# Kernel optimization log

Measured on AMD Instinct MI355X. Metric: run time of the kernel, lower is better.

## Reference

```python
import jax, jax.numpy as jnp
import numpy as np

B, S, D = 2, 2048, 2048
H, G, HD = 16, 8, 128          # query heads, kv groups, head_dim
GS = H // G                     # group size (queries per kv head)
EPS = 1e-6


def _rmsnorm(x, scale):
    # Qwen3-compatible: upcast to f32, rms over last dim, scale
    xf = x.astype(jnp.float32)
    ms = jnp.mean(xf * xf, axis=-1, keepdims=True)
    return (xf * jax.lax.rsqrt(ms + EPS) * scale).astype(x.dtype)


def _rope(x, cos, sin):
    # x: (b, h, s, hd); cos/sin: (s, hd) rotate-half convention
    hd = x.shape[-1]
    x1, x2 = x[..., : hd // 2], x[..., hd // 2 :]
    rotated = jnp.concatenate([-x2, x1], axis=-1)
    s = x.shape[2]
    c = cos[None, None, :s, :]
    sn = sin[None, None, :s, :]
    return (x * c + rotated * sn).astype(x.dtype)


def setup_inputs() -> dict:
    key = jax.random.key(0)
    ks = jax.random.split(key, 8)
    x = jax.random.normal(ks[0], (B, S, D), jnp.float32)
    # causal mask: True = masked (future positions)
    mask = jnp.triu(jnp.ones((S, S), dtype=bool), k=1)
    # RoPE tables, rotate-half convention (cat(angles, angles))
    inv_freq = 1.0 / (10000.0 ** (np.arange(0, HD, 2, dtype=np.float32) / HD))
    angles = np.arange(S, dtype=np.float32)[:, None] * inv_freq[None, :]
    angles = np.concatenate([angles, angles], axis=-1)  # (S, HD)
    cos = jnp.asarray(np.cos(angles))
    sin = jnp.asarray(np.sin(angles))
    std = 0.02
    Wq = jax.random.normal(ks[1], (D, H * HD), jnp.float32) * std
    Wk = jax.random.normal(ks[2], (D, G * HD), jnp.float32) * std
    Wv = jax.random.normal(ks[3], (D, G * HD), jnp.float32) * std
    Wo = jax.random.normal(ks[4], (H * HD, D), jnp.float32) * std
    q_scale = jnp.ones((HD,), jnp.float32)
    k_scale = jnp.ones((HD,), jnp.float32)
    return {"x": x, "mask": mask, "cos": cos, "sin": sin,
            "Wq": Wq, "Wk": Wk, "Wv": Wv, "Wo": Wo,
            "q_scale": q_scale, "k_scale": k_scale}


def reference(x, mask, cos, sin, Wq, Wk, Wv, Wo, q_scale, k_scale):
    b, s, _ = x.shape
    q = (x @ Wq).reshape(b, s, H, HD).transpose(0, 2, 1, 3)   # (b,H,s,hd)
    k = (x @ Wk).reshape(b, s, G, HD).transpose(0, 2, 1, 3)   # (b,G,s,hd)
    v = (x @ Wv).reshape(b, s, G, HD).transpose(0, 2, 1, 3)   # (b,G,s,hd)
    q = _rmsnorm(q, q_scale)
    k = _rmsnorm(k, k_scale)
    q = _rope(q, cos, sin)
    k = _rope(k, cos, sin)
    # grouped attention: avoid repeat_interleave by grouping query heads
    qg = q.reshape(b, G, GS, s, HD)
    scores = jnp.einsum('bghqd,bgkd->bghqk', qg, k)           # (b,G,GS,s,s)
    scores = jnp.where(mask[None, None, None, :, :], -jnp.inf, scores)
    weights = jax.nn.softmax(scores / jnp.sqrt(jnp.float32(HD)), axis=-1)
    ctx = jnp.einsum('bghqk,bgkd->bghqd', weights, v)          # (b,G,GS,s,hd)
    ctx = ctx.reshape(b, H, s, HD).transpose(0, 2, 1, 3).reshape(b, s, H * HD)
    return ctx @ Wo
```

## Files before the change

### kernel.cpp

```cpp
#include <hip/hip_runtime.h>
#include <stdint.h>

#define S_LEN 2048
#define NH 16
#define NG 8
#define HDIM 128

typedef __bf16 bf16x8 __attribute__((ext_vector_type(8)));
typedef __bf16 bf16x4v __attribute__((ext_vector_type(4)));
typedef float f32x4 __attribute__((ext_vector_type(4)));

#define MFMA16(a, b, c) __builtin_amdgcn_mfma_f32_16x16x32_bf16((a), (b), (c), 0, 0, 0)

__device__ __forceinline__ uint16_t f2bf(float f) {
  union { float f; uint32_t u; } v; v.f = f;
  return (uint16_t)((v.u + 0x7fffu + ((v.u >> 16) & 1u)) >> 16);
}

__device__ __forceinline__ void gload16(const void* g, void* l) {
  __builtin_amdgcn_global_load_lds(
      (__attribute__((address_space(1))) const void*)g,
      (__attribute__((address_space(3))) void*)l, 16, 0, 0);
}

__global__ __launch_bounds__(256) void cvt_x_kernel(
    const float* __restrict__ x, uint16_t* __restrict__ xb, int n4) {
  int i = blockIdx.x * 256 + threadIdx.x;
  if (i >= n4) return;
  float4 v = ((const float4*)x)[i];
  ushort4 o;
  o.x = f2bf(v.x); o.y = f2bf(v.y); o.z = f2bf(v.z); o.w = f2bf(v.w);
  ((ushort4*)xb)[i] = o;
}

__global__ __launch_bounds__(256) void trans_cvt_kernel(
    const float* __restrict__ src, uint16_t* __restrict__ dst, int K, int N) {
  __shared__ float T[32][33];
  int n0 = blockIdx.x * 32, k0 = blockIdx.y * 32;
  int tx = threadIdx.x & 31, ty = threadIdx.x >> 5;
  #pragma unroll
  for (int i = 0; i < 4; ++i)
    T[ty + i * 8][tx] = src[(size_t)(k0 + ty + i * 8) * N + n0 + tx];
  __syncthreads();
  #pragma unroll
  for (int i = 0; i < 4; ++i)
    dst[(size_t)(n0 + ty + i * 8) * K + k0 + tx] = f2bf(T[tx][ty + i * 8]);
}

template <int NISSUE>
__device__ __forceinline__ void stage_half(const uint16_t* __restrict__ g,
                                           int ldg, char* lds, int tid) {
  #pragma unroll
  for (int i = 0; i < NISSUE; ++i) {
    int ch = i * 512 + tid;
    int pair = ch >> 3, slotd = ch & 7;
    int slotl = slotd ^ (pair & 7);
    int row = pair * 2 + (slotl >> 2), c2 = slotl & 3;
    gload16(g + (size_t)row * ldg + c2 * 8, lds + ch * 16);
  }
}

__device__ __forceinline__ bf16x8 ldsfrag(const char* half_base, int row, int l4) {
  int pair = row >> 1;
  int slot = ((row & 1) << 2) | l4;
  return *(const bf16x8*)(half_base + pair * 128 + ((slot ^ (pair & 7)) * 16));
}

#define BAR() asm volatile("s_barrier" ::: "memory")

template <int BM>
__global__ __launch_bounds__(512, 2) void gemm8p_kernel(
    const uint16_t* __restrict__ A, const uint16_t* __restrict__ BT,
    float* __restrict__ C, int M, int N, int K, int gridN) {
  extern __shared__ char smem[];
  constexpr int MI = BM / 32;
  constexpr int LA = BM / 128;
  constexpr int ABYTES = BM * 64;
  const int tid = threadIdx.x, lane = tid & 63;
  const int wid = tid >> 6;
  const int l15 = lane & 15, l4 = lane >> 4;
  const int wm = wid >> 2, wn = wid & 3;

  const int nwg = gridDim.x, bid = blockIdx.x;
  const int cpx = nwg >> 3;
  const int swz = (bid & 7) * cpx + (bid >> 3);
  const int m0 = (swz / gridN) * BM, n0 = (swz % gridN) * 256;

  const uint16_t* Ag = A + (size_t)m0 * K;
  const uint16_t* Bg = BT + (size_t)n0 * K;
  const int NT = K >> 6;

#define ABASE(p, k) (smem + (((p) << 1) | (k)) * ABYTES)
#define BBASE(p, k) (smem + 4 * ABYTES + (((p) << 1) | (k)) * 16384)

  f32x4 acc[MI][4];
  #pragma unroll
  for (int mi = 0; mi < MI; ++mi)
    #pragma unroll
    for (int ni = 0; ni < 4; ++ni) acc[mi][ni] = (f32x4){0.f, 0.f, 0.f, 0.f};

  stage_half<LA>(Ag, K, ABASE(0, 0), tid);
  stage_half<2>(Bg, K, BBASE(0, 0), tid);
  stage_half<LA>(Ag + 32, K, ABASE(0, 1), tid);
  stage_half<2>(Bg + 32, K, BBASE(0, 1), tid);
  stage_half<LA>(Ag + 64, K, ABASE(1, 0), tid);
  stage_half<2>(Bg + 64, K, BBASE(1, 0), tid);
  if constexpr (BM == 256) asm volatile("s_waitcnt vmcnt(4)" ::: "memory");
  else                     asm volatile("s_waitcnt vmcnt(3)" ::: "memory");
  BAR();

  int par = 0;
  const int arow = wm * (BM / 2) + l15;
  for (int u = 0; u < NT; ++u, par ^= 1) {
    const int k0 = u * 64;
    bf16x8 af[MI], bf0, bf1;
    #pragma unroll
    for (int mi = 0; mi < MI; ++mi) af[mi] = ldsfrag(ABASE(par, 0), arow + mi * 16, l4);
    bf0 = ldsfrag(BBASE(par, 0), wn * 64 + l15, l4);
    bf1 = ldsfrag(BBASE(par, 0), wn * 64 + 16 + l15, l4);
    if (u + 1 < NT) stage_half<LA>(Ag + (k0 + 96), K, ABASE(par ^ 1, 1), tid);
    BAR();
    __builtin_amdgcn_s_setprio(1);
    #pragma unroll
    for (int mi = 0; mi < MI; ++mi) {
      acc[mi][0] = MFMA16(af[mi], bf0, acc[mi][0]);
      acc[mi][1] = MFMA16(af[mi], bf1, acc[mi][1]);
    }
    __builtin_amdgcn_s_setprio(0);
    BAR();
    bf0 = ldsfrag(BBASE(par, 0), wn * 64 + 32 + l15, l4);
    bf1 = ldsfrag(BBASE(par, 0), wn * 64 + 48 + l15, l4);
    if (u + 1 < NT) stage_half<2>(Bg + (k0 + 96), K, BBASE(par ^ 1, 1), tid);
    BAR();
    __builtin_amdgcn_s_setprio(1);
    #pragma unroll
    for (int mi = 0; mi < MI; ++mi) {
      acc[mi][2] = MFMA16(af[mi], bf0, acc[mi][2]);
      acc[mi][3] = MFMA16(af[mi], bf1, acc[mi][3]);
    }
    __builtin_amdgcn_s_setprio(0);
    BAR();
    #pragma unroll
    for (int mi = 0; mi < MI; ++mi) af[mi] = ldsfrag(ABASE(par, 1), arow + mi * 16, l4);
    bf0 = ldsfrag(BBASE(par, 1), wn * 64 + 32 + l15, l4);
    bf1 = ldsfrag(BBASE(par, 1), wn * 64 + 48 + l15, l4);
    if (u + 2 < NT) stage_half<LA>(Ag + (k0 + 128), K, ABASE(par, 0), tid);
    BAR();
    __builtin_amdgcn_s_setprio(1);
    #pragma unroll
    for (int mi = 0; mi < MI; ++mi) {
      acc[mi][2] = MFMA16(af[mi], bf0, acc[mi][2]);
      acc[mi][3] = MFMA16(af[mi], bf1, acc[mi][3]);
    }
    __builtin_amdgcn_s_setprio(0);
    BAR();
    bf0 = ldsfrag(BBASE(par, 1), wn * 64 + l15, l4);
    bf1 = ldsfrag(BBASE(par, 1), wn * 64 + 16 + l15, l4);
    if (u + 2 < NT) stage_half<2>(Bg + (k0 + 128), K, BBASE(par, 0), tid);
    BAR();
    __builtin_amdgcn_s_setprio(1);
    #pragma unroll
    for (int mi = 0; mi < MI; ++mi) {
      acc[mi][0] = MFMA16(af[mi], bf0, acc[mi][0]);
      acc[mi][1] = MFMA16(af[mi], bf1, acc[mi][1]);
    }
    __builtin_amdgcn_s_setprio(0);
    if (u + 2 < NT) {
      if constexpr (BM == 256) asm volatile("s_waitcnt vmcnt(4)" ::: "memory");
      else                     asm volatile("s_waitcnt vmcnt(3)" ::: "memory");
    } else {
      asm volatile("s_waitcnt vmcnt(0)" ::: "memory");
    }
    BAR();
  }

  #pragma unroll
  for (int mi = 0; mi < MI; ++mi)
    #pragma unroll
    for (int ni = 0; ni < 4; ++ni) {
      float* dst = C + (size_t)(m0 + wm * (BM / 2) + mi * 16 + l4 * 4) * N +
                   n0 + wn * 64 + ni * 16 + l15;
      #pragma unroll
      for (int r = 0; r < 4; ++r) dst[(size_t)r * N] = acc[mi][ni][r];
    }
#undef ABASE
#undef BBASE
}

__global__ __launch_bounds__(256) void qk_rope_kernel(
    const float* __restrict__ QKV, const float* __restrict__ cosb,
    const float* __restrict__ sinb, const float* __restrict__ qs,
    const float* __restrict__ ks, uint16_t* __restrict__ Qb,
    uint16_t* __restrict__ Kb) {
  const int task = blockIdx.x * 4 + (threadIdx.x >> 6);
  const int lane = threadIdx.x & 63;
  const int hh = task % 24;
  const int row = task / 24;
  const int s = row & (S_LEN - 1);
  const int b = row >> 11;
  const float c1 = cosb[s * 128 + lane], c2 = cosb[s * 128 + 64 + lane];
  const float s1 = sinb[s * 128 + lane], s2 = sinb[s * 128 + 64 + lane];
  const float* src = QKV + (size_t)row * 4096;
  float v1, v2, sc1, sc2, outscale;
  uint16_t* dst;
  if (hh < 16) {
    v1 = src[hh * 128 + lane]; v2 = src[hh * 128 + 64 + lane];
    sc1 = qs[lane]; sc2 = qs[lane + 64];
    outscale = 0.088388347648318447f;
    dst = Qb + ((size_t)(b * NH + hh) * S_LEN + s) * 128;
  } else {
    int g = hh - 16;
    v1 = src[2048 + g * 128 + lane]; v2 = src[2048 + g * 128 + 64 + lane];
    sc1 = ks[lane]; sc2 = ks[lane + 64];
    outscale = 1.0f;
    dst = Kb + ((size_t)(b * NG + g) * S_LEN + s) * 128;
  }
  float ss = v1 * v1 + v2 * v2;
  #pragma unroll
  for (int o = 1; o < 64; o <<= 1) ss += __shfl_xor(ss, o);
  float inv = rsqrtf(ss * (1.0f / 128.0f) + 1e-6f);
  float n1 = v1 * inv * sc1, n2 = v2 * inv * sc2;
  dst[lane] = f2bf((n1 * c1 - n2 * s1) * outscale);
  dst[lane + 64] = f2bf((n2 * c2 + n1 * s2) * outscale);
}

__global__ __launch_bounds__(256) void v_trans_kernel(
    const float* __restrict__ QKV, uint16_t* __restrict__ Vt) {
  __shared__ uint16_t T[128][72];
  const int s0 = blockIdx.x * 64;
  const int bg = blockIdx.y;
  const int b = bg >> 3, g = bg & 7;
  const int tid = threadIdx.x;
  const int tc = tid & 127, tr = tid >> 7;
  const float* src = QKV + ((size_t)(b * S_LEN + s0)) * 4096 + 3072 + g * 128;
  #pragma unroll
  for (int i = 0; i < 32; ++i) {
    int r = i * 2 + tr;
    T[tc][r] = f2bf(src[(size_t)r * 4096 + tc]);
  }
  __syncthreads();
  uint16_t* dst = Vt + (size_t)bg * 128 * S_LEN + s0;
  #pragma unroll
  for (int i = 0; i < 32; ++i) {
    int idx = i * 256 + tid;
    int d = idx >> 6, sof = idx & 63;
    dst[(size_t)d * S_LEN + sof] = T[d][sof];
  }
}

__global__ __launch_bounds__(512) void attn_kernel(
    const uint16_t* __restrict__ Qb, const uint16_t* __restrict__ Kb,
    const uint16_t* __restrict__ Vt, uint16_t* __restrict__ Ctx) {
  __shared__ uint8_t smem[65536 + 8 * 2304];
  const int tid = threadIdx.x, lane = tid & 63, wid = tid >> 6;
  uint16_t* Ps = (uint16_t*)(smem + 65536) + wid * 1152;
  const int l15 = lane & 15, l4 = lane >> 4;

  const int bg = blockIdx.y;
  const int b = bg >> 3, g = bg & 7;
  const int h = (g << 1) | (wid >> 2);
  const int bh = b * NH + h;

  const uint16_t* Qh = Qb + (size_t)bh * S_LEN * HDIM;
  const uint16_t* Kh = Kb + (size_t)bg * S_LEN * HDIM;
  const uint16_t* Vh = Vt + (size_t)bg * HDIM * S_LEN;

  const int k_row = lane >> 4, k_c = lane & 15;
  const int v_row = lane >> 3, v_c = lane & 7;

#define STAGE(kt_, buf_)                                                      \
  do {                                                                        \
    const int kv0_ = (kt_) * 64;                                              \
    uint16_t* KsB_ = (uint16_t*)(smem + (buf_) * 16384);                      \
    uint16_t* VsB_ = (uint16_t*)(smem + 32768 + (buf_) * 16384);              \
    _Pragma("unroll")                                                         \
    for (int i_ = 0; i_ < 2; ++i_) {                                          \
      int chunk_ = wid * 2 + i_;                                              \
      int row_ = chunk_ * 4 + k_row;                                          \
      int sc_ = (k_c ^ (row_ & 7)) * 8;                                       \
      gload16(Kh + (size_t)(kv0_ + row_) * HDIM + sc_, KsB_ + chunk_ * 512);  \
    }                                                                         \
    _Pragma("unroll")                                                         \
    for (int i_ = 0; i_ < 2; ++i_) {                                          \
      int chunk_ = wid * 2 + i_;                                              \
      int row_ = chunk_ * 8 + v_row;                                          \
      int sc_ = (v_c ^ (row_ & 7)) * 8;                                       \
      gload16(Vh + (size_t)row_ * S_LEN + kv0_ + sc_, VsB_ + chunk_ * 512);   \
    }                                                                         \
  } while (0)

  for (int half = 0; half < 2; ++half) {
    const int qtile = half ? (31 - (int)blockIdx.x) : (int)blockIdx.x;
    const int q0 = qtile * 64;
    const int qrow = q0 + (wid & 3) * 16 + l15;

    bf16x8 qf[4];
    #pragma unroll
    for (int kk = 0; kk < 4; ++kk)
      qf[kk] = *(const bf16x8*)(Qh + (size_t)qrow * HDIM + kk * 32 + l4 * 8);

    f32x4 acc[8];
    #pragma unroll
    for (int i = 0; i < 8; ++i) acc[i] = (f32x4){0.f, 0.f, 0.f, 0.f};
    float mrun = -1e30f, lrun = 0.f;

    const int nt = qtile + 1;
    int cur = 0;
    STAGE(0, 0);
    asm volatile("s_waitcnt vmcnt(0)\ns_barrier" ::: "memory");

    for (int kt = 0; kt < nt; ++kt) {
      const int kv0 = kt * 64;
      if (kt + 1 < nt) STAGE(kt + 1, cur ^ 1);

      uint16_t* Ks = (uint16_t*)(smem + cur * 16384);
      uint16_t* Vs = (uint16_t*)(smem + 32768 + cur * 16384);

      f32x4 sc[4];
      #pragma unroll
      for (int i = 0; i < 4; ++i) sc[i] = (f32x4){0.f, 0.f, 0.f, 0.f};
      __builtin_amdgcn_s_setprio(1);
      #pragma unroll
      for (int kk = 0; kk < 4; ++kk) {
        #pragma unroll
        for (int kc = 0; kc < 4; ++kc) {
          int key = kc * 16 + l15;
          int cc = (kk * 4 + l4) ^ (key & 7);
          bf16x8 kf = *(const bf16x8*)(Ks + key * 128 + cc * 8);
          sc[kc] = MFMA16(kf, qf[kk], sc[kc]);
        }
      }
      __builtin_amdgcn_s_setprio(0);
      if (kt == nt - 1) {
        #pragma unroll
        for (int kc = 0; kc < 4; ++kc)
          #pragma unroll
          for (int r = 0; r < 4; ++r)
            if (kv0 + kc * 16 + l4 * 4 + r > qrow) sc[kc][r] = -1e30f;
      }
      float tmax = -1e30f;
      #pragma unroll
      for (int kc = 0; kc < 4; ++kc)
        #pragma unroll
        for (int r = 0; r < 4; ++r) tmax = fmaxf(tmax, sc[kc][r]);
      tmax = fmaxf(tmax, __shfl_xor(tmax, 16));
      tmax = fmaxf(tmax, __shfl_xor(tmax, 32));
      if (!__all(tmax <= mrun + 8.0f)) {
        float mnew = fmaxf(mrun, tmax);
        float corr = __expf(mrun - mnew);
        lrun *= corr;
        #pragma unroll
        for (int d0 = 0; d0 < 8; ++d0) acc[d0] *= corr;
        mrun = mnew;
      }
      float tsum = 0.f;
      #pragma unroll
      for (int kc = 0; kc < 4; ++kc) {
        float p0 = __expf(sc[kc][0] - mrun);
        float p1 = __expf(sc[kc][1] - mrun);
        float p2 = __expf(sc[kc][2] - mrun);
        float p3 = __expf(sc[kc][3] - mrun);
        tsum += (p0 + p1) + (p2 + p3);
        bf16x4v pw = {(__bf16)p0, (__bf16)p1, (__bf16)p2, (__bf16)p3};
        *(bf16x4v*)(Ps + l15 * 72 + kc * 16 + l4 * 4) = pw;
      }
      tsum += __shfl_xor(tsum, 16);
      tsum += __shfl_xor(tsum, 32);
      lrun += tsum;

      __builtin_amdgcn_s_setprio(1);
      #pragma unroll
      for (int hf = 0; hf < 2; ++hf) {
        bf16x8 pf = *(const bf16x8*)(Ps + l15 * 72 + hf * 32 + l4 * 8);
        #pragma unroll
        for (int d0 = 0; d0 < 8; ++d0) {
          int d = d0 * 16 + l15;
          int cc = (hf * 4 + l4) ^ (d & 7);
          bf16x8 vf = *(const bf16x8*)(Vs + d * 64 + cc * 8);
          acc[d0] = MFMA16(vf, pf, acc[d0]);
        }
      }
      __builtin_amdgcn_s_setprio(0);

      asm volatile("s_waitcnt vmcnt(0)\ns_barrier" ::: "memory");
      cur ^= 1;
    }

    float inv = 1.0f / lrun;
    uint16_t* dst = Ctx + ((size_t)(b * S_LEN + qrow) * NH + h) * HDIM;
    #pragma unroll
    for (int d0 = 0; d0 < 8; ++d0) {
      bf16x4v o = {(__bf16)(acc[d0][0] * inv), (__bf16)(acc[d0][1] * inv),
                   (__bf16)(acc[d0][2] * inv), (__bf16)(acc[d0][3] * inv)};
      *(bf16x4v*)(dst + d0 * 16 + l4 * 4) = o;
    }
  }
#undef STAGE
}

extern "C" void kernel_launch(void* const* d_in, const int* in_sizes, int n_in,
                              void* d_out, int out_size, void* d_ws, size_t ws_size,
                              hipStream_t stream) {
  const float* x    = (const float*)d_in[0];
  const float* cosb = (const float*)d_in[2];
  const float* sinb = (const float*)d_in[3];
  const float* Wq   = (const float*)d_in[4];
  const float* Wk   = (const float*)d_in[5];
  const float* Wv   = (const float*)d_in[6];
  const float* Wo   = (const float*)d_in[7];
  const float* qs   = (const float*)d_in[8];
  const float* ks   = (const float*)d_in[9];

  char* ws = (char*)d_ws;
  uint16_t* Xb    = (uint16_t*)(ws);
  uint16_t* WallT = (uint16_t*)(ws + (16ull << 20));
  uint16_t* WoT   = (uint16_t*)(ws + (32ull << 20));
  float*    QKV   = (float*)   (ws + (40ull << 20));
  uint16_t* Qb    = (uint16_t*)(ws + (104ull << 20));
  uint16_t* Kb    = (uint16_t*)(ws + (120ull << 20));
  uint16_t* Vt    = (uint16_t*)(ws + (128ull << 20));
  uint16_t* Ctx   = (uint16_t*)(ws + (136ull << 20));
  float* out = (float*)d_out;

  hipFuncSetAttribute(reinterpret_cast<const void*>(&gemm8p_kernel<256>),
                      hipFuncAttributeMaxDynamicSharedMemorySize, 131072);
  hipFuncSetAttribute(reinterpret_cast<const void*>(&gemm8p_kernel<128>),
                      hipFuncAttributeMaxDynamicSharedMemorySize, 98304);

  cvt_x_kernel<<<8192, 256, 0, stream>>>(x, Xb, 2097152);
  trans_cvt_kernel<<<dim3(64, 64), 256, 0, stream>>>(Wq, WallT, 2048, 2048);
  trans_cvt_kernel<<<dim3(32, 64), 256, 0, stream>>>(Wk, WallT + 2048 * 2048, 2048, 1024);
  trans_cvt_kernel<<<dim3(32, 64), 256, 0, stream>>>(Wv, WallT + 3072 * 2048, 2048, 1024);
  trans_cvt_kernel<<<dim3(64, 64), 256, 0, stream>>>(Wo, WoT, 2048, 2048);
  gemm8p_kernel<256><<<256, 512, 131072, stream>>>(Xb, WallT, QKV, 4096, 4096, 2048, 16);
  qk_rope_kernel<<<24576, 256, 0, stream>>>(QKV, cosb, sinb, qs, ks, Qb, Kb);
  v_trans_kernel<<<dim3(32, 16), 256, 0, stream>>>(QKV, Vt);
  attn_kernel<<<dim3(16, 16), 512, 0, stream>>>(Qb, Kb, Vt, Ctx);
  gemm8p_kernel<128><<<256, 512, 98304, stream>>>(Ctx, WoT, out, 4096, 2048, 2048, 8);
}
```

Baseline: 341.8 us.

## Restructure GEMM main loop to two phases per iteration with precomputed offsets

Rewrites the bf16 GEMM main loop from four barrier-separated quarter-steps into two half-steps per iteration. Each half-step issues A and B global->LDS loads together, then loads all A/B fragments and runs the full MI x 4 MFMA block. Global and LDS address offsets are precomputed once per thread to cut integer address math. Fewer barriers and larger MFMA bursts should reduce sync overhead, but the wait counts change and register pressure rises from holding four B fragments.

```diff
diff --git a/kernel.cpp b/kernel.cpp
--- a/kernel.cpp
+++ b/kernel.cpp
@@ -47,25 +47,6 @@
     dst[(size_t)(n0 + ty + i * 8) * K + k0 + tx] = f2bf(T[tx][ty + i * 8]);
 }
 
-template <int NISSUE>
-__device__ __forceinline__ void stage_half(const uint16_t* __restrict__ g,
-                                           int ldg, char* lds, int tid) {
-  #pragma unroll
-  for (int i = 0; i < NISSUE; ++i) {
-    int ch = i * 512 + tid;
-    int pair = ch >> 3, slotd = ch & 7;
-    int slotl = slotd ^ (pair & 7);
-    int row = pair * 2 + (slotl >> 2), c2 = slotl & 3;
-    gload16(g + (size_t)row * ldg + c2 * 8, lds + ch * 16);
-  }
-}
-
-__device__ __forceinline__ bf16x8 ldsfrag(const char* half_base, int row, int l4) {
-  int pair = row >> 1;
-  int slot = ((row & 1) << 2) | l4;
-  return *(const bf16x8*)(half_base + pair * 128 + ((slot ^ (pair & 7)) * 16));
-}
-
 #define BAR() asm volatile("s_barrier" ::: "memory")
 
 template <int BM>
@@ -76,6 +57,7 @@
   constexpr int MI = BM / 32;
   constexpr int LA = BM / 128;
   constexpr int ABYTES = BM * 64;
+  constexpr int BOFF = 4 * ABYTES;
   const int tid = threadIdx.x, lane = tid & 63;
   const int wid = tid >> 6;
   const int l15 = lane & 15, l4 = lane >> 4;
@@ -90,8 +72,60 @@
   const uint16_t* Bg = BT + (size_t)n0 * K;
   const int NT = K >> 6;
 
-#define ABASE(p, k) (smem + (((p) << 1) | (k)) * ABYTES)
-#define BBASE(p, k) (smem + 4 * ABYTES + (((p) << 1) | (k)) * 16384)
+  size_t gAo[LA]; int lAo[LA];
+  #pragma unroll
+  for (int i = 0; i < LA; ++i) {
+    int ch = i * 512 + tid;
+    int pair = ch >> 3, slotd = ch & 7;
+    int slotl = slotd ^ (pair & 7);
+    int row = pair * 2 + (slotl >> 2), c2 = slotl & 3;
+    gAo[i] = (size_t)row * K + c2 * 8;
+    lAo[i] = ch * 16;
+  }
+  size_t gBo[2]; int lBo[2];
+  #pragma unroll
+  for (int i = 0; i < 2; ++i) {
+    int ch = i * 512 + tid;
+    int pair = ch >> 3, slotd = ch & 7;
+    int slotl = slotd ^ (pair & 7);
+    int row = pair * 2 + (slotl >> 2), c2 = slotl & 3;
+    gBo[i] = (size_t)row * K + c2 * 8;
+    lBo[i] = ch * 16;
+  }
+  const int arow = wm * (BM / 2) + l15;
+  int aoff[MI];
+  #pragma unroll
+  for (int mi = 0; mi < MI; ++mi) {
+    int r = arow + mi * 16;
+    int pair = r >> 1, slot = ((r & 1) << 2) | l4;
+    aoff[mi] = pair * 128 + ((slot ^ (pair & 7)) * 16);
+  }
+  int boff[4];
+  #pragma unroll
+  for (int ni = 0; ni < 4; ++ni) {
+    int r = wn * 64 + ni * 16 + l15;
+    int pair = r >> 1, slot = ((r & 1) << 2) | l4;
+    boff[ni] = pair * 128 + ((slot ^ (pair & 7)) * 16);
+  }
+
+#define STAGE_A(koff, slot)                                                   \
+  do {                                                                        \
+    _Pragma("unroll")                                                         \
+    for (int i_ = 0; i_ < LA; ++i_)                                           \
+      gload16(Ag + gAo[i_] + (koff), smem + (slot)*ABYTES + lAo[i_]);         \
+  } while (0)
+#define STAGE_B(koff, slot)                                                   \
+  do {                                                                        \
+    _Pragma("unroll")                                                         \
+    for (int i_ = 0; i_ < 2; ++i_)                                            \
+      gload16(Bg + gBo[i_] + (koff), smem + BOFF + (slot)*16384 + lBo[i_]);   \
+  } while (0)
+#define WAIT_STEADY()                                                         \
+  do { if constexpr (BM == 256) asm volatile("s_waitcnt vmcnt(8)" ::: "memory"); \
+       else                     asm volatile("s_waitcnt vmcnt(6)" ::: "memory"); } while (0)
+#define WAIT_TAIL0()                                                          \
+  do { if constexpr (BM == 256) asm volatile("s_waitcnt vmcnt(4)" ::: "memory"); \
+       else                     asm volatile("s_waitcnt vmcnt(3)" ::: "memory"); } while (0)
 
   f32x4 acc[MI][4];
   #pragma unroll
@@ -99,79 +133,57 @@
     #pragma unroll
     for (int ni = 0; ni < 4; ++ni) acc[mi][ni] = (f32x4){0.f, 0.f, 0.f, 0.f};
 
-  stage_half<LA>(Ag, K, ABASE(0, 0), tid);
-  stage_half<2>(Bg, K, BBASE(0, 0), tid);
-  stage_half<LA>(Ag + 32, K, ABASE(0, 1), tid);
-  stage_half<2>(Bg + 32, K, BBASE(0, 1), tid);
-  stage_half<LA>(Ag + 64, K, ABASE(1, 0), tid);
-  stage_half<2>(Bg + 64, K, BBASE(1, 0), tid);
-  if constexpr (BM == 256) asm volatile("s_waitcnt vmcnt(4)" ::: "memory");
-  else                     asm volatile("s_waitcnt vmcnt(3)" ::: "memory");
-  BAR();
+  STAGE_A(0, 0);  STAGE_B(0, 0);
+  STAGE_A(32, 1); STAGE_B(32, 1);
+  STAGE_A(64, 2); STAGE_B(64, 2);
 
   int par = 0;
-  const int arow = wm * (BM / 2) + l15;
   for (int u = 0; u < NT; ++u, par ^= 1) {
-    const int k0 = u * 64;
-    bf16x8 af[MI], bf0, bf1;
-    #pragma unroll
-    for (int mi = 0; mi < MI; ++mi) af[mi] = ldsfrag(ABASE(par, 0), arow + mi * 16, l4);
-    bf0 = ldsfrag(BBASE(par, 0), wn * 64 + l15, l4);
-    bf1 = ldsfrag(BBASE(par, 0), wn * 64 + 16 + l15, l4);
-    if (u + 1 < NT) stage_half<LA>(Ag + (k0 + 96), K, ABASE(par ^ 1, 1), tid);
+    const int kb = u * 64;
+    bf16x8 af[MI], bfr[4];
+    if (u == NT - 1) WAIT_TAIL0(); else WAIT_STEADY();
     BAR();
+    if (u + 1 < NT) {
+      STAGE_A(kb + 96, 2 * (par ^ 1) + 1);
+      STAGE_B(kb + 96, 2 * (par ^ 1) + 1);
+    }
+    {
+      const char* Ab = smem + (2 * par + 0) * ABYTES;
+      const char* Bb = smem + BOFF + (2 * par + 0) * 16384;
+      #pragma unroll
+      for (int mi = 0; mi < MI; ++mi) af[mi] = *(const bf16x8*)(Ab + aoff[mi]);
+      #pragma unroll
+      for (int ni = 0; ni < 4; ++ni) bfr[ni] = *(const bf16x8*)(Bb + boff[ni]);
+    }
     __builtin_amdgcn_s_setprio(1);
     #pragma unroll
-    for (int mi = 0; mi < MI; ++mi) {
-      acc[mi][0] = MFMA16(af[mi], bf0, acc[mi][0]);
-      acc[mi][1] = MFMA16(af[mi], bf1, acc[mi][1]);
-    }
+    for (int mi = 0; mi < MI; ++mi)
+      #pragma unroll
+      for (int ni = 0; ni < 4; ++ni)
+        acc[mi][ni] = MFMA16(af[mi], bfr[ni], acc[mi][ni]);
     __builtin_amdgcn_s_setprio(0);
+    if (u == NT - 1) asm volatile("s_waitcnt vmcnt(0)" ::: "memory");
+    else WAIT_STEADY();
     BAR();
-    bf0 = ldsfrag(BBASE(par, 0), wn * 64 + 32 + l15, l4);
-    bf1 = ldsfrag(BBASE(par, 0), wn * 64 + 48 + l15, l4);
-    if (u + 1 < NT) stage_half<2>(Bg + (k0 + 96), K, BBASE(par ^ 1, 1), tid);
-    BAR();
+    if (u + 2 < NT) {
+      STAGE_A(kb + 128, 2 * par + 0);
+      STAGE_B(kb + 128, 2 * par + 0);
+    }
+    {
+      const char* Ab = smem + (2 * par + 1) * ABYTES;
+      const char* Bb = smem + BOFF + (2 * par + 1) * 16384;
+      #pragma unroll
+      for (int mi = 0; mi < MI; ++mi) af[mi] = *(const bf16x8*)(Ab + aoff[mi]);
+      #pragma unroll
+      for (int ni = 0; ni < 4; ++ni) bfr[ni] = *(const bf16x8*)(Bb + boff[ni]);
+    }
     __builtin_amdgcn_s_setprio(1);
     #pragma unroll
-    for (int mi = 0; mi < MI; ++mi) {
-      acc[mi][2] = MFMA16(af[mi], bf0, acc[mi][2]);
-      acc[mi][3] = MFMA16(af[mi], bf1, acc[mi][3]);
-    }
+    for (int mi = 0; mi < MI; ++mi)
+      #pragma unroll
+      for (int ni = 0; ni < 4; ++ni)
+        acc[mi][ni] = MFMA16(af[mi], bfr[ni], acc[mi][ni]);
     __builtin_amdgcn_s_setprio(0);
-    BAR();
-    #pragma unroll
-    for (int mi = 0; mi < MI; ++mi) af[mi] = ldsfrag(ABASE(par, 1), arow + mi * 16, l4);
-    bf0 = ldsfrag(BBASE(par, 1), wn * 64 + 32 + l15, l4);
-    bf1 = ldsfrag(BBASE(par, 1), wn * 64 + 48 + l15, l4);
-    if (u + 2 < NT) stage_half<LA>(Ag + (k0 + 128), K, ABASE(par, 0), tid);
-    BAR();
-    __builtin_amdgcn_s_setprio(1);
-    #pragma unroll
-    for (int mi = 0; mi < MI; ++mi) {
-      acc[mi][2] = MFMA16(af[mi], bf0, acc[mi][2]);
-      acc[mi][3] = MFMA16(af[mi], bf1, acc[mi][3]);
-    }
-    __builtin_amdgcn_s_setprio(0);
-    BAR();
-    bf0 = ldsfrag(BBASE(par, 1), wn * 64 + l15, l4);
-    bf1 = ldsfrag(BBASE(par, 1), wn * 64 + 16 + l15, l4);
-    if (u + 2 < NT) stage_half<2>(Bg + (k0 + 128), K, BBASE(par, 0), tid);
-    BAR();
-    __builtin_amdgcn_s_setprio(1);
-    #pragma unroll
-    for (int mi = 0; mi < MI; ++mi) {
-      acc[mi][0] = MFMA16(af[mi], bf0, acc[mi][0]);
-      acc[mi][1] = MFMA16(af[mi], bf1, acc[mi][1]);
-    }
-    __builtin_amdgcn_s_setprio(0);
-    if (u + 2 < NT) {
-      if constexpr (BM == 256) asm volatile("s_waitcnt vmcnt(4)" ::: "memory");
-      else                     asm volatile("s_waitcnt vmcnt(3)" ::: "memory");
-    } else {
-      asm volatile("s_waitcnt vmcnt(0)" ::: "memory");
-    }
-    BAR();
   }
 
   #pragma unroll
@@ -183,8 +195,10 @@
       #pragma unroll
       for (int r = 0; r < 4; ++r) dst[(size_t)r * N] = acc[mi][ni][r];
     }
-#undef ABASE
-#undef BBASE
+#undef STAGE_A
+#undef STAGE_B
+#undef WAIT_STEADY
+#undef WAIT_TAIL0
 }
 
 __global__ __launch_bounds__(256) void qk_rope_kernel(
```

Result: no change. 342.0 us (+0.1%).
